# Kernel tuning notes

Measured on AMD Instinct MI355X. Metric: run time of the kernel, lower is better.

## Reference

```python
import jax, jax.numpy as jnp
import numpy as np

EPS = 1e-8
THRESHOLD = 0.2

def setup_inputs() -> dict:
    key = jax.random.key(0)
    k1, k2 = jax.random.split(key)
    N, D, H = 8192, 256, 2
    x = jax.random.normal(k1, (N, D), dtype=jnp.float32)
    # per-head elementwise metric weight (MetricCalcLayer.weight, xavier-uniform init)
    bound = float(np.sqrt(6.0 / (1 + D)))
    w = jax.random.uniform(k2, (H, D), dtype=jnp.float32, minval=-bound, maxval=bound)
    K = 81  # int(N * 0.01), resolved top-k count per row
    return {"x": x, "w": w, "K": K}

def reference(x, w, K):
    # x: [N, D], w: [H, D]
    H = w.shape[0]
    N = x.shape[0]
    wx = x[None, :, :] * w[:, None, :]                       # [H, N, D]
    norms = jnp.linalg.norm(wx, axis=-1, keepdims=True)      # [H, N, 1]
    wn = wx / jnp.maximum(norms, EPS)                        # normalized per head
    # sum of per-head cosine similarity matrices, averaged over heads
    sim = jnp.einsum('hnd,hmd->nm', wn, wn) / H              # [N, N]
    # threshold (reverse=False): zero out entries below threshold
    sim = jnp.where(sim < THRESHOLD, jnp.zeros_like(sim), sim)
    # top-k per row -> scatter ones into a mask, multiply
    _, idx = jax.lax.top_k(sim, K)                           # [N, K]
    mask = jnp.zeros_like(sim).at[jnp.arange(N)[:, None], idx].set(1.0)
    return sim * mask
```

## Files before the change

### kernel.cpp

```cpp
#include <hip/hip_runtime.h>
#include <hip/hip_bf16.h>
#include <stdint.h>

#define NROWS 8192
#define DIM   256
#define KDIM  512
#define THRESH 0.2f
#define MARGIN 0.005f
#define BLK_FIX_CAP 512
#define TOPK_CAP 4096

typedef __bf16 bf16x8 __attribute__((ext_vector_type(8)));
typedef float  f32x4  __attribute__((ext_vector_type(4)));
typedef float  f32x2  __attribute__((ext_vector_type(2)));

__device__ __forceinline__ void gload16(const void* g, void* l) {
  __builtin_amdgcn_global_load_lds(
      (const __attribute__((address_space(1))) uint32_t*)g,
      (__attribute__((address_space(3))) uint32_t*)l,
      16, 0, 0);
}

__global__ __launch_bounds__(256) void prep_k(const float* __restrict__ x,
                                              const float* __restrict__ w,
                                              ushort* __restrict__ z,
                                              int* __restrict__ cnt) {
  const int wv = threadIdx.x >> 6, lane = threadIdx.x & 63;
  const int n = blockIdx.x * 4 + wv;
  if (lane == 0) cnt[n] = 0;
  const int d4 = lane * 4;
  const f32x4 xv = *(const f32x4*)&x[(size_t)n * DIM + d4];
  const f32x4 w0 = *(const f32x4*)&w[d4];
  const f32x4 w1 = *(const f32x4*)&w[DIM + d4];
  f32x4 p0, p1;
  float s0 = 0.f, s1 = 0.f;
  #pragma unroll
  for (int j = 0; j < 4; ++j) {
    p0[j] = xv[j] * w0[j];  s0 += p0[j] * p0[j];
    p1[j] = xv[j] * w1[j];  s1 += p1[j] * p1[j];
  }
  #pragma unroll
  for (int off = 32; off > 0; off >>= 1) {
    s0 += __shfl_xor(s0, off);
    s1 += __shfl_xor(s1, off);
  }
  const float inv0 = 0.70710678118654752f / fmaxf(sqrtf(s0), 1e-8f);
  const float inv1 = 0.70710678118654752f / fmaxf(sqrtf(s1), 1e-8f);
  ushort4 o0, o1;
  {
    __hip_bfloat16 b;
    b = __float2bfloat16(p0[0] * inv0); o0.x = *(ushort*)&b;
    b = __float2bfloat16(p0[1] * inv0); o0.y = *(ushort*)&b;
    b = __float2bfloat16(p0[2] * inv0); o0.z = *(ushort*)&b;
    b = __float2bfloat16(p0[3] * inv0); o0.w = *(ushort*)&b;
    b = __float2bfloat16(p1[0] * inv1); o1.x = *(ushort*)&b;
    b = __float2bfloat16(p1[1] * inv1); o1.y = *(ushort*)&b;
    b = __float2bfloat16(p1[2] * inv1); o1.z = *(ushort*)&b;
    b = __float2bfloat16(p1[3] * inv1); o1.w = *(ushort*)&b;
  }
  *(ushort4*)&z[(size_t)n * KDIM + d4]       = o0;
  *(ushort4*)&z[(size_t)n * KDIM + DIM + d4] = o1;
}

__global__ __launch_bounds__(256, 4) void sim_gemm(const ushort* __restrict__ z,
                                               const float* __restrict__ x,
                                               const float* __restrict__ w,
                                               float* __restrict__ out,
                                               int* __restrict__ cnt) {
  const int u = blockIdx.x;
  int bm = (int)((129.0 - sqrt(129.0 * 129.0 - 8.0 * (double)u)) * 0.5);
  if (bm > 63) bm = 63;
  while (bm * (129 - bm) / 2 > u) --bm;
  while ((bm + 1) * (129 - (bm + 1)) / 2 <= u) ++bm;
  const int bn = bm + (u - bm * (129 - bm) / 2);
  const bool offd = (bm != bn);

  __shared__ __align__(16) char smem[33280];
  ushort* ASb = (ushort*)smem;
  ushort* BSb = (ushort*)(smem + 16384);
  auto T2 = (float (*)[32][130])smem;
  __shared__ int cntA[128], cntB[128];
  __shared__ uint32_t fix_loc[BLK_FIX_CAP];
  __shared__ int fix_loc_n;

  const int t = threadIdx.x;
  const int rowA = bm * 128, rowB = bn * 128;
  const int wv = t >> 6, lane = t & 63;
  const int wr = wv >> 1, wc = wv & 1;

  f32x4 acc[4][4];
  #pragma unroll
  for (int i = 0; i < 4; ++i)
    #pragma unroll
    for (int j = 0; j < 4; ++j) acc[i][j] = (f32x4)0.f;

  int aoff[4], boff[4];
  #pragma unroll
  for (int mi = 0; mi < 4; ++mi) {
    const int ar = wr * 64 + mi * 16 + (lane & 15);
    const int sw = (lane >> 4) ^ ((ar >> 1) & 3);
    aoff[mi] = ar * 32 + sw * 8;
  }
  #pragma unroll
  for (int ni = 0; ni < 4; ++ni) {
    const int br = wc * 64 + ni * 16 + (lane & 15);
    const int sw = (lane >> 4) ^ ((br >> 1) & 3);
    boff[ni] = br * 32 + sw * 8;
  }

  if (t < 128) { cntA[t] = 0; cntB[t] = 0; }
  if (t == 0) fix_loc_n = 0;

  const int i0 = t, r0 = i0 >> 2, s0_ = i0 & 3, cs0 = s0_ ^ ((r0 >> 1) & 3);
  const int i1 = t + 256, r1 = i1 >> 2, s1_ = i1 & 3, cs1 = s1_ ^ ((r1 >> 1) & 3);
  const ushort* zA0 = z + (size_t)(rowA + r0) * KDIM + cs0 * 8;
  const ushort* zB0 = z + (size_t)(rowB + r0) * KDIM + cs0 * 8;
  const ushort* zA1 = z + (size_t)(rowA + r1) * KDIM + cs1 * 8;
  const ushort* zB1 = z + (size_t)(rowB + r1) * KDIM + cs1 * 8;

  gload16(zA0,      ASb + (size_t)i0 * 8);
  gload16(zB0,      BSb + (size_t)i0 * 8);
  gload16(zA1,      ASb + (size_t)i1 * 8);
  gload16(zB1,      BSb + (size_t)i1 * 8);
  gload16(zA0 + 32, ASb + 4096 + (size_t)i0 * 8);
  gload16(zB0 + 32, BSb + 4096 + (size_t)i0 * 8);
  gload16(zA1 + 32, ASb + 4096 + (size_t)i1 * 8);
  gload16(zB1 + 32, BSb + 4096 + (size_t)i1 * 8);

  int cur = 0;
#define KSTEP(VMWAIT, STAGE_KB)                                                   \
  {                                                                               \
    asm volatile("s_waitcnt " VMWAIT ::: "memory");                               \
    __builtin_amdgcn_s_barrier();                                                 \
    __builtin_amdgcn_sched_barrier(0);                                            \
    const ushort* Ac = ASb + cur * 4096;                                          \
    const ushort* Bc = BSb + cur * 4096;                                          \
    bf16x8 af[4], bfv[4];                                                         \
    _Pragma("unroll")                                                             \
    for (int mi = 0; mi < 4; ++mi) af[mi] = *(const bf16x8*)(Ac + aoff[mi]);      \
    _Pragma("unroll")                                                             \
    for (int ni = 0; ni < 4; ++ni) bfv[ni] = *(const bf16x8*)(Bc + boff[ni]);     \
    asm volatile("s_waitcnt lgkmcnt(0)" ::: "memory");                            \
    __builtin_amdgcn_sched_barrier(0);                                            \
    __builtin_amdgcn_s_barrier();                                                 \
    __builtin_amdgcn_sched_barrier(0);                                            \
    if ((STAGE_KB) >= 0) {                                                        \
      const int kb = (STAGE_KB);                                                  \
      ushort* An = ASb + cur * 4096;                                              \
      ushort* Bn = BSb + cur * 4096;                                              \
      gload16(zA0 + kb, An + (size_t)i0 * 8);                                     \
      gload16(zB0 + kb, Bn + (size_t)i0 * 8);                                     \
      gload16(zA1 + kb, An + (size_t)i1 * 8);                                     \
      gload16(zB1 + kb, Bn + (size_t)i1 * 8);                                     \
    }                                                                             \
    _Pragma("unroll")                                                             \
    for (int mi = 0; mi < 4; ++mi)                                                \
      _Pragma("unroll")                                                           \
      for (int ni = 0; ni < 4; ++ni)                                              \
        acc[mi][ni] = __builtin_amdgcn_mfma_f32_16x16x32_bf16(af[mi], bfv[ni],    \
                                                              acc[mi][ni], 0, 0, 0); \
    cur ^= 1;                                                                     \
  }

  for (int kt = 0; kt < 14; ++kt) KSTEP("vmcnt(4)", (kt + 2) * 32);
  KSTEP("vmcnt(4)", -1);
  KSTEP("vmcnt(0)", -1);
#undef KSTEP

  #pragma unroll
  for (int mi = 0; mi < 4; ++mi) {
    #pragma unroll
    for (int ni = 0; ni < 4; ++ni) {
      const f32x4 v = acc[mi][ni];
      const int lc = wc * 64 + ni * 16 + (lane & 15);
      const int gc = rowB + lc;
      const int lrbase = wr * 64 + mi * 16 + (lane >> 4) * 4;
      #pragma unroll
      for (int r = 0; r < 4; ++r) {
        const float val = v[r];
        const int lr = lrbase + r;
        out[(size_t)(rowA + lr) * NROWS + gc] = (val < THRESH) ? 0.0f : val;
        if (val >= THRESH - MARGIN) {
          atomicAdd(&cntA[lr], 1);
          if (offd) atomicAdd(&cntB[lc], 1);
          if (val < THRESH + MARGIN) {
            const int p = atomicAdd(&fix_loc_n, 1);
            if (p < BLK_FIX_CAP) fix_loc[p] = (uint32_t)(rowA + lr) * NROWS + gc;
          }
        }
      }
    }
  }

  if (offd) {
    #pragma unroll
    for (int p = 0; p < 2; ++p) {
      __syncthreads();
      {
        #pragma unroll
        for (int ni2 = 0; ni2 < 2; ++ni2) {
          const int ni = p * 2 + ni2;
          const int tc = ni2 * 16 + (lane & 15);
          #pragma unroll
          for (int mi = 0; mi < 4; ++mi) {
            const int lrb = wr * 64 + mi * 16 + (lane >> 4) * 4;
            #pragma unroll
            for (int r = 0; r < 4; ++r) T2[wc][tc][lrb + r] = acc[mi][ni][r];
          }
        }
      }
      __syncthreads();
      #pragma unroll
      for (int h = 0; h < 2; ++h) {
        const int c = p + 2 * h;
        #pragma unroll
        for (int it = 0; it < 8; ++it) {
          const int j = it * 4 + wv;
          const int i = (t & 63) * 2;
          f32x2 v2 = *(const f32x2*)&T2[h][j][i];
          v2.x = (v2.x < THRESH) ? 0.0f : v2.x;
          v2.y = (v2.y < THRESH) ? 0.0f : v2.y;
          __builtin_nontemporal_store(v2,
              (f32x2*)&out[(size_t)(rowB + c * 32 + j) * NROWS + rowA + i]);
        }
      }
    }
  }
  __syncthreads();

  {
    const int nf = (fix_loc_n < BLK_FIX_CAP) ? fix_loc_n : BLK_FIX_CAP;
    for (int e = wv; e < nf; e += 4) {
      const uint32_t f = fix_loc[e];
      const int r = (int)(f / NROWS), c = (int)(f % NROWS);
      double dot0 = 0, dot1 = 0, nr0 = 0, nr1 = 0, nc0 = 0, nc1 = 0;
      #pragma unroll
      for (int i2 = 0; i2 < DIM / 64; ++i2) {
        const int i = i2 * 64 + lane;
        const double w0 = (double)w[i],              w1 = (double)w[DIM + i];
        const double xr = (double)x[(size_t)r * DIM + i];
        const double xc = (double)x[(size_t)c * DIM + i];
        const double pr0 = xr * w0, pc0 = xc * w0;
        const double pr1 = xr * w1, pc1 = xc * w1;
        dot0 += pr0 * pc0; nr0 += pr0 * pr0; nc0 += pc0 * pc0;
        dot1 += pr1 * pc1; nr1 += pr1 * pr1; nc1 += pc1 * pc1;
      }
      #pragma unroll
      for (int off = 32; off > 0; off >>= 1) {
        dot0 += __shfl_down(dot0, off); nr0 += __shfl_down(nr0, off); nc0 += __shfl_down(nc0, off);
        dot1 += __shfl_down(dot1, off); nr1 += __shfl_down(nr1, off); nc1 += __shfl_down(nc1, off);
      }
      if (lane == 0) {
        const double s0 = dot0 / (fmax(sqrt(nr0), 1e-8) * fmax(sqrt(nc0), 1e-8));
        const double s1 = dot1 / (fmax(sqrt(nr1), 1e-8) * fmax(sqrt(nc1), 1e-8));
        const double sim = 0.5 * (s0 + s1);
        const float res = (sim < (double)THRESH) ? 0.0f : (float)sim;
        out[(size_t)r * NROWS + c] = res;
        out[(size_t)c * NROWS + r] = res;
      }
    }
  }

  if (t < 128) {
    if (cntA[t] > 0) atomicAdd(&cnt[rowA + t], cntA[t]);
    if (offd && cntB[t] > 0) atomicAdd(&cnt[rowB + t], cntB[t]);
  }
}

__global__ __launch_bounds__(256) void topk_fix(float* __restrict__ out,
                                                const int* __restrict__ cnt,
                                                const int* __restrict__ Kp) {
  const int K = Kp[0];
  __shared__ float vals[TOPK_CAP];
  __shared__ int   idxs[TOPK_CAP];
  __shared__ int   num;
  for (int rr = 0; rr < 8; ++rr) {
    const int row = blockIdx.x * 8 + rr;
    if (cnt[row] <= K) continue;

    if (threadIdx.x == 0) num = 0;
    __syncthreads();
    for (int j = threadIdx.x; j < NROWS; j += 256) {
      const float v = out[(size_t)row * NROWS + j];
      if (v != 0.0f) {
        const int p = atomicAdd(&num, 1);
        if (p < TOPK_CAP) { vals[p] = v; idxs[p] = j; }
      }
    }
    __syncthreads();
    const int c = (num < TOPK_CAP) ? num : TOPK_CAP;
    for (int p = threadIdx.x; p < c; p += 256) {
      const float v = vals[p];
      const int  id = idxs[p];
      int rank = 0;
      for (int q = 0; q < c; ++q) {
        const float u = vals[q];
        rank += (u > v) || (u == v && idxs[q] < id);
      }
      if (rank >= K) out[(size_t)row * NROWS + id] = 0.0f;
    }
    __syncthreads();
  }
}

extern "C" void kernel_launch(void* const* d_in, const int* in_sizes, int n_in,
                              void* d_out, int out_size, void* d_ws, size_t ws_size,
                              hipStream_t stream) {
  const float* x  = (const float*)d_in[0];
  const float* w  = (const float*)d_in[1];
  const int*   Kp = (const int*)d_in[2];
  float* out = (float*)d_out;

  char* ws = (char*)d_ws;
  ushort* z   = (ushort*)ws;
  int*    cnt = (int*)(ws + (size_t)NROWS * KDIM * 2);

  prep_k<<<NROWS / 4, 256, 0, stream>>>(x, w, z, cnt);
  sim_gemm<<<2080, 256, 0, stream>>>(z, x, w, out, cnt);
  topk_fix<<<NROWS / 8, 256, 0, stream>>>(out, cnt, Kp);
}
```

Before: 118.3 us.

## Process two triangular tiles per block and prefetch the second tile's operands

The similarity GEMM now launches half as many blocks, and each block loops over two upper-triangular tiles, u and u+1040. After the first tile's epilogue barrier, it issues the first k-slab loads for the second tile so they overlap with the first tile's fix-up recomputation and count atomics. The aim is to hide the prologue load latency and cut per-block launch overhead. In exchange, each block runs serially over twice the work, and shared state such as counters and the fix list must be re-initialised between tiles, which adds an extra barrier.

```diff
diff --git a/kernel.cpp b/kernel.cpp
--- a/kernel.cpp
+++ b/kernel.cpp
@@ -9,6 +9,8 @@
 #define MARGIN 0.005f
 #define BLK_FIX_CAP 512
 #define TOPK_CAP 4096
+#define NTILE 2080
+#define GRID_P 1040
 
 typedef __bf16 bf16x8 __attribute__((ext_vector_type(8)));
 typedef float  f32x4  __attribute__((ext_vector_type(4)));
@@ -19,6 +21,14 @@
       (const __attribute__((address_space(1))) uint32_t*)g,
       (__attribute__((address_space(3))) uint32_t*)l,
       16, 0, 0);
+}
+
+__device__ __forceinline__ void tri_decode(int u, int& bm, int& bn) {
+  bm = (int)((129.0 - sqrt(129.0 * 129.0 - 8.0 * (double)u)) * 0.5);
+  if (bm > 63) bm = 63;
+  while (bm * (129 - bm) / 2 > u) --bm;
+  while ((bm + 1) * (129 - (bm + 1)) / 2 <= u) ++bm;
+  bn = bm + (u - bm * (129 - bm) / 2);
 }
 
 __global__ __launch_bounds__(256) void prep_k(const float* __restrict__ x,
@@ -67,14 +77,6 @@
                                                const float* __restrict__ w,
                                                float* __restrict__ out,
                                                int* __restrict__ cnt) {
-  const int u = blockIdx.x;
-  int bm = (int)((129.0 - sqrt(129.0 * 129.0 - 8.0 * (double)u)) * 0.5);
-  if (bm > 63) bm = 63;
-  while (bm * (129 - bm) / 2 > u) --bm;
-  while ((bm + 1) * (129 - (bm + 1)) / 2 <= u) ++bm;
-  const int bn = bm + (u - bm * (129 - bm) / 2);
-  const bool offd = (bm != bn);
-
   __shared__ __align__(16) char smem[33280];
   ushort* ASb = (ushort*)smem;
   ushort* BSb = (ushort*)(smem + 16384);
@@ -84,15 +86,15 @@
   __shared__ int fix_loc_n;
 
   const int t = threadIdx.x;
-  const int rowA = bm * 128, rowB = bn * 128;
   const int wv = t >> 6, lane = t & 63;
   const int wr = wv >> 1, wc = wv & 1;
 
-  f32x4 acc[4][4];
-  #pragma unroll
-  for (int i = 0; i < 4; ++i)
-    #pragma unroll
-    for (int j = 0; j < 4; ++j) acc[i][j] = (f32x4)0.f;
+  const int i0 = t, r0 = i0 >> 2, s0_ = i0 & 3, cs0 = s0_ ^ ((r0 >> 1) & 3);
+  const int i1 = t + 256, r1 = i1 >> 2, s1_ = i1 & 3, cs1 = s1_ ^ ((r1 >> 1) & 3);
+
+  int bm0, bn0, bm1, bn1;
+  tri_decode(blockIdx.x, bm0, bn0);
+  tri_decode(blockIdx.x + GRID_P, bm1, bn1);
 
   int aoff[4], boff[4];
   #pragma unroll
@@ -108,26 +110,42 @@
     boff[ni] = br * 32 + sw * 8;
   }
 
-  if (t < 128) { cntA[t] = 0; cntB[t] = 0; }
-  if (t == 0) fix_loc_n = 0;
-
-  const int i0 = t, r0 = i0 >> 2, s0_ = i0 & 3, cs0 = s0_ ^ ((r0 >> 1) & 3);
-  const int i1 = t + 256, r1 = i1 >> 2, s1_ = i1 & 3, cs1 = s1_ ^ ((r1 >> 1) & 3);
-  const ushort* zA0 = z + (size_t)(rowA + r0) * KDIM + cs0 * 8;
-  const ushort* zB0 = z + (size_t)(rowB + r0) * KDIM + cs0 * 8;
-  const ushort* zA1 = z + (size_t)(rowA + r1) * KDIM + cs1 * 8;
-  const ushort* zB1 = z + (size_t)(rowB + r1) * KDIM + cs1 * 8;
-
-  gload16(zA0,      ASb + (size_t)i0 * 8);
-  gload16(zB0,      BSb + (size_t)i0 * 8);
-  gload16(zA1,      ASb + (size_t)i1 * 8);
-  gload16(zB1,      BSb + (size_t)i1 * 8);
-  gload16(zA0 + 32, ASb + 4096 + (size_t)i0 * 8);
-  gload16(zB0 + 32, BSb + 4096 + (size_t)i0 * 8);
-  gload16(zA1 + 32, ASb + 4096 + (size_t)i1 * 8);
-  gload16(zB1 + 32, BSb + 4096 + (size_t)i1 * 8);
-
-  int cur = 0;
+  {
+    const int rowA = bm0 * 128, rowB = bn0 * 128;
+    const ushort* zA0 = z + (size_t)(rowA + r0) * KDIM + cs0 * 8;
+    const ushort* zB0 = z + (size_t)(rowB + r0) * KDIM + cs0 * 8;
+    const ushort* zA1 = z + (size_t)(rowA + r1) * KDIM + cs1 * 8;
+    const ushort* zB1 = z + (size_t)(rowB + r1) * KDIM + cs1 * 8;
+    gload16(zA0,      ASb + (size_t)i0 * 8);
+    gload16(zB0,      BSb + (size_t)i0 * 8);
+    gload16(zA1,      ASb + (size_t)i1 * 8);
+    gload16(zB1,      BSb + (size_t)i1 * 8);
+    gload16(zA0 + 32, ASb + 4096 + (size_t)i0 * 8);
+    gload16(zB0 + 32, BSb + 4096 + (size_t)i0 * 8);
+    gload16(zA1 + 32, ASb + 4096 + (size_t)i1 * 8);
+    gload16(zB1 + 32, BSb + 4096 + (size_t)i1 * 8);
+  }
+
+  for (int tt = 0; tt < 2; ++tt) {
+    const int bm = tt ? bm1 : bm0, bn = tt ? bn1 : bn0;
+    const bool offd = (bm != bn);
+    const int rowA = bm * 128, rowB = bn * 128;
+    const ushort* zA0 = z + (size_t)(rowA + r0) * KDIM + cs0 * 8;
+    const ushort* zB0 = z + (size_t)(rowB + r0) * KDIM + cs0 * 8;
+    const ushort* zA1 = z + (size_t)(rowA + r1) * KDIM + cs1 * 8;
+    const ushort* zB1 = z + (size_t)(rowB + r1) * KDIM + cs1 * 8;
+
+    if (tt) __syncthreads();
+    if (t < 128) { cntA[t] = 0; cntB[t] = 0; }
+    if (t == 0) fix_loc_n = 0;
+
+    f32x4 acc[4][4];
+    #pragma unroll
+    for (int i = 0; i < 4; ++i)
+      #pragma unroll
+      for (int j = 0; j < 4; ++j) acc[i][j] = (f32x4)0.f;
+
+    int cur = 0;
 #define KSTEP(VMWAIT, STAGE_KB)                                                   \
   {                                                                               \
     asm volatile("s_waitcnt " VMWAIT ::: "memory");                               \
@@ -162,108 +180,125 @@
     cur ^= 1;                                                                     \
   }
 
-  for (int kt = 0; kt < 14; ++kt) KSTEP("vmcnt(4)", (kt + 2) * 32);
-  KSTEP("vmcnt(4)", -1);
-  KSTEP("vmcnt(0)", -1);
+    for (int kt = 0; kt < 14; ++kt) KSTEP("vmcnt(4)", (kt + 2) * 32);
+    KSTEP("vmcnt(4)", -1);
+    KSTEP("vmcnt(0)", -1);
 #undef KSTEP
 
-  #pragma unroll
-  for (int mi = 0; mi < 4; ++mi) {
     #pragma unroll
-    for (int ni = 0; ni < 4; ++ni) {
-      const f32x4 v = acc[mi][ni];
-      const int lc = wc * 64 + ni * 16 + (lane & 15);
-      const int gc = rowB + lc;
-      const int lrbase = wr * 64 + mi * 16 + (lane >> 4) * 4;
+    for (int mi = 0; mi < 4; ++mi) {
       #pragma unroll
-      for (int r = 0; r < 4; ++r) {
-        const float val = v[r];
-        const int lr = lrbase + r;
-        out[(size_t)(rowA + lr) * NROWS + gc] = (val < THRESH) ? 0.0f : val;
-        if (val >= THRESH - MARGIN) {
-          atomicAdd(&cntA[lr], 1);
-          if (offd) atomicAdd(&cntB[lc], 1);
-          if (val < THRESH + MARGIN) {
-            const int p = atomicAdd(&fix_loc_n, 1);
-            if (p < BLK_FIX_CAP) fix_loc[p] = (uint32_t)(rowA + lr) * NROWS + gc;
+      for (int ni = 0; ni < 4; ++ni) {
+        const f32x4 v = acc[mi][ni];
+        const int lc = wc * 64 + ni * 16 + (lane & 15);
+        const int gc = rowB + lc;
+        const int lrbase = wr * 64 + mi * 16 + (lane >> 4) * 4;
+        #pragma unroll
+        for (int r = 0; r < 4; ++r) {
+          const float val = v[r];
+          const int lr = lrbase + r;
+          out[(size_t)(rowA + lr) * NROWS + gc] = (val < THRESH) ? 0.0f : val;
+          if (val >= THRESH - MARGIN) {
+            atomicAdd(&cntA[lr], 1);
+            if (offd) atomicAdd(&cntB[lc], 1);
+            if (val < THRESH + MARGIN) {
+              const int p = atomicAdd(&fix_loc_n, 1);
+              if (p < BLK_FIX_CAP) fix_loc[p] = (uint32_t)(rowA + lr) * NROWS + gc;
+            }
           }
         }
       }
     }
-  }
-
-  if (offd) {
-    #pragma unroll
-    for (int p = 0; p < 2; ++p) {
-      __syncthreads();
-      {
+
+    if (offd) {
+      #pragma unroll
+      for (int p = 0; p < 2; ++p) {
+        __syncthreads();
+        {
+          #pragma unroll
+          for (int ni2 = 0; ni2 < 2; ++ni2) {
+            const int ni = p * 2 + ni2;
+            const int tc = ni2 * 16 + (lane & 15);
+            #pragma unroll
+            for (int mi = 0; mi < 4; ++mi) {
+              const int lrb = wr * 64 + mi * 16 + (lane >> 4) * 4;
+              #pragma unroll
+              for (int r = 0; r < 4; ++r) T2[wc][tc][lrb + r] = acc[mi][ni][r];
+            }
+          }
+        }
+        __syncthreads();
         #pragma unroll
-        for (int ni2 = 0; ni2 < 2; ++ni2) {
-          const int ni = p * 2 + ni2;
-          const int tc = ni2 * 16 + (lane & 15);
+        for (int h = 0; h < 2; ++h) {
+          const int c = p + 2 * h;
           #pragma unroll
-          for (int mi = 0; mi < 4; ++mi) {
-            const int lrb = wr * 64 + mi * 16 + (lane >> 4) * 4;
-            #pragma unroll
-            for (int r = 0; r < 4; ++r) T2[wc][tc][lrb + r] = acc[mi][ni][r];
+          for (int it = 0; it < 8; ++it) {
+            const int j = it * 4 + wv;
+            const int i = (t & 63) * 2;
+            f32x2 v2 = *(const f32x2*)&T2[h][j][i];
+            v2.x = (v2.x < THRESH) ? 0.0f : v2.x;
+            v2.y = (v2.y < THRESH) ? 0.0f : v2.y;
+            __builtin_nontemporal_store(v2,
+                (f32x2*)&out[(size_t)(rowB + c * 32 + j) * NROWS + rowA + i]);
           }
         }
       }
-      __syncthreads();
-      #pragma unroll
-      for (int h = 0; h < 2; ++h) {
-        const int c = p + 2 * h;
+    }
+    __syncthreads();
+
+    if (tt == 0) {
+      const int rA1 = bm1 * 128, rB1 = bn1 * 128;
+      const ushort* nA0 = z + (size_t)(rA1 + r0) * KDIM + cs0 * 8;
+      const ushort* nB0 = z + (size_t)(rB1 + r0) * KDIM + cs0 * 8;
+      const ushort* nA1 = z + (size_t)(rA1 + r1) * KDIM + cs1 * 8;
+      const ushort* nB1 = z + (size_t)(rB1 + r1) * KDIM + cs1 * 8;
+      gload16(nA0,      ASb + (size_t)i0 * 8);
+      gload16(nB0,      BSb + (size_t)i0 * 8);
+      gload16(nA1,      ASb + (size_t)i1 * 8);
+      gload16(nB1,      BSb + (size_t)i1 * 8);
+      gload16(nA0 + 32, ASb + 4096 + (size_t)i0 * 8);
+      gload16(nB0 + 32, BSb + 4096 + (size_t)i0 * 8);
+      gload16(nA1 + 32, ASb + 4096 + (size_t)i1 * 8);
+      gload16(nB1 + 32, BSb + 4096 + (size_t)i1 * 8);
+    }
+
+    {
+      const int nf = (fix_loc_n < BLK_FIX_CAP) ? fix_loc_n : BLK_FIX_CAP;
+      for (int e = wv; e < nf; e += 4) {
+        const uint32_t f = fix_loc[e];
+        const int r = (int)(f / NROWS), c = (int)(f % NROWS);
+        double dot0 = 0, dot1 = 0, nr0 = 0, nr1 = 0, nc0 = 0, nc1 = 0;
         #pragma unroll
-        for (int it = 0; it < 8; ++it) {
-          const int j = it * 4 + wv;
-          const int i = (t & 63) * 2;
-          f32x2 v2 = *(const f32x2*)&T2[h][j][i];
-          v2.x = (v2.x < THRESH) ? 0.0f : v2.x;
-          v2.y = (v2.y < THRESH) ? 0.0f : v2.y;
-          __builtin_nontemporal_store(v2,
-              (f32x2*)&out[(size_t)(rowB + c * 32 + j) * NROWS + rowA + i]);
-        }
-      }
-    }
-  }
-  __syncthreads();
-
-  {
-    const int nf = (fix_loc_n < BLK_FIX_CAP) ? fix_loc_n : BLK_FIX_CAP;
-    for (int e = wv; e < nf; e += 4) {
-      const uint32_t f = fix_loc[e];
-      const int r = (int)(f / NROWS), c = (int)(f % NROWS);
-      double dot0 = 0, dot1 = 0, nr0 = 0, nr1 = 0, nc0 = 0, nc1 = 0;
-      #pragma unroll
-      for (int i2 = 0; i2 < DIM / 64; ++i2) {
-        const int i = i2 * 64 + lane;
-        const double w0 = (double)w[i],              w1 = (double)w[DIM + i];
-        const double xr = (double)x[(size_t)r * DIM + i];
-        const double xc = (double)x[(size_t)c * DIM + i];
-        const double pr0 = xr * w0, pc0 = xc * w0;
-        const double pr1 = xr * w1, pc1 = xc * w1;
-        dot0 += pr0 * pc0; nr0 += pr0 * pr0; nc0 += pc0 * pc0;
-        dot1 += pr1 * pc1; nr1 += pr1 * pr1; nc1 += pc1 * pc1;
-      }
-      #pragma unroll
-      for (int off = 32; off > 0; off >>= 1) {
-        dot0 += __shfl_down(dot0, off); nr0 += __shfl_down(nr0, off); nc0 += __shfl_down(nc0, off);
-        dot1 += __shfl_down(dot1, off); nr1 += __shfl_down(nr1, off); nc1 += __shfl_down(nc1, off);
-      }
-      if (lane == 0) {
-        const double s0 = dot0 / (fmax(sqrt(nr0), 1e-8) * fmax(sqrt(nc0), 1e-8));
-        const double s1 = dot1 / (fmax(sqrt(nr1), 1e-8) * fmax(sqrt(nc1), 1e-8));
-        const double sim = 0.5 * (s0 + s1);
-        const float res = (sim < (double)THRESH) ? 0.0f : (float)sim;
-        out[(size_t)r * NROWS + c] = res;
-        out[(size_t)c * NROWS + r] = res;
-      }
-    }
-  }
-
-  if (t < 128) {
-    if (cntA[t] > 0) atomicAdd(&cnt[rowA + t], cntA[t]);
-    if (offd && cntB[t] > 0) atomicAdd(&cnt[rowB + t], cntB[t]);
+        for (int i2 = 0; i2 < DIM / 64; ++i2) {
+          const int i = i2 * 64 + lane;
+          const double w0 = (double)w[i],              w1 = (double)w[DIM + i];
+          const double xr = (double)x[(size_t)r * DIM + i];
+          const double xc = (double)x[(size_t)c * DIM + i];
+          const double pr0 = xr * w0, pc0 = xc * w0;
+          const double pr1 = xr * w1, pc1 = xc * w1;
+          dot0 += pr0 * pc0; nr0 += pr0 * pr0; nc0 += pc0 * pc0;
+          dot1 += pr1 * pc1; nr1 += pr1 * pr1; nc1 += pc1 * pc1;
+        }
+        #pragma unroll
+        for (int off = 32; off > 0; off >>= 1) {
+          dot0 += __shfl_down(dot0, off); nr0 += __shfl_down(nr0, off); nc0 += __shfl_down(nc0, off);
+          dot1 += __shfl_down(dot1, off); nr1 += __shfl_down(nr1, off); nc1 += __shfl_down(nc1, off);
+        }
+        if (lane == 0) {
+          const double s0 = dot0 / (fmax(sqrt(nr0), 1e-8) * fmax(sqrt(nc0), 1e-8));
+          const double s1 = dot1 / (fmax(sqrt(nr1), 1e-8) * fmax(sqrt(nc1), 1e-8));
+          const double sim = 0.5 * (s0 + s1);
+          const float res = (sim < (double)THRESH) ? 0.0f : (float)sim;
+          out[(size_t)r * NROWS + c] = res;
+          out[(size_t)c * NROWS + r] = res;
+        }
+      }
+    }
+
+    if (t < 128) {
+      if (cntA[t] > 0) atomicAdd(&cnt[rowA + t], cntA[t]);
+      if (offd && cntB[t] > 0) atomicAdd(&cnt[rowB + t], cntB[t]);
+    }
   }
 }
 
@@ -316,6 +351,6 @@
   int*    cnt = (int*)(ws + (size_t)NROWS * KDIM * 2);
 
   prep_k<<<NROWS / 4, 256, 0, stream>>>(x, w, z, cnt);
-  sim_gemm<<<2080, 256, 0, stream>>>(z, x, w, out, cnt);
+  sim_gemm<<<GRID_P, 256, 0, stream>>>(z, x, w, out, cnt);
   topk_fix<<<NROWS / 8, 256, 0, stream>>>(out, cnt, Kp);
 }
```

After: 192.3 us. 62.5% more time.
